# Performance work log

Hardware: AMD Instinct MI355X
Metric: run time of the kernel (lower is better)

## Reference

```python
import jax, jax.numpy as jnp
import numpy as np

B, T, I, H, O = 256, 2048, 6, 64, 6  # batch, time, input_dim, hidden_dim, output_dim


def setup_inputs() -> dict:
    key = jax.random.key(0)
    ks = jax.random.split(key, 11)
    s = 0.1  # param init scale
    return {
        "x": jax.random.normal(ks[0], (B, T, I), jnp.float32),
        # LSTM layer 0 (gate order i, f, g, o as in PyTorch; b = b_ih + b_hh)
        "Wih0": jax.random.normal(ks[1], (4 * H, I), jnp.float32) * s,
        "Whh0": jax.random.normal(ks[2], (4 * H, H), jnp.float32) * s,
        "b0": jax.random.normal(ks[3], (4 * H,), jnp.float32) * s,
        # LSTM layer 1
        "Wih1": jax.random.normal(ks[4], (4 * H, H), jnp.float32) * s,
        "Whh1": jax.random.normal(ks[5], (4 * H, H), jnp.float32) * s,
        "b1": jax.random.normal(ks[6], (4 * H,), jnp.float32) * s,
        # FC head
        "W1": jax.random.normal(ks[7], (H, H), jnp.float32) * s,
        "bf1": jax.random.normal(ks[8], (H,), jnp.float32) * s,
        "W2": jax.random.normal(ks[9], (O, H), jnp.float32) * s,
        "bf2": jax.random.normal(ks[10], (O,), jnp.float32) * s,
    }


def lstm_layer(x, Wih, Whh, b):
    """Single LSTM layer, batch_first. x: (B, T, F) -> (B, T, H)."""
    h_dim = Whh.shape[1]
    # precompute input contribution to gates for all timesteps: (B, T, 4H)
    xg = jnp.einsum('btf,gf->btg', x, Wih) + b

    def step(carry, xg_t):
        h, c = carry
        g = xg_t + h @ Whh.T                      # (B, 4H)
        i, f, gg, o = jnp.split(g, 4, axis=-1)    # PyTorch gate order i,f,g,o
        i = jax.nn.sigmoid(i)
        f = jax.nn.sigmoid(f)
        gg = jnp.tanh(gg)
        o = jax.nn.sigmoid(o)
        c = f * c + i * gg
        h = o * jnp.tanh(c)
        return (h, c), h

    h0 = jnp.zeros((x.shape[0], h_dim), x.dtype)
    _, hs = jax.lax.scan(step, (h0, h0), jnp.swapaxes(xg, 0, 1))  # (T, B, H)
    return jnp.swapaxes(hs, 0, 1)


def reference(x, Wih0, Whh0, b0, Wih1, Whh1, b1, W1, bf1, W2, bf2):
    h = lstm_layer(x, Wih0, Whh0, b0)
    h = lstm_layer(h, Wih1, Whh1, b1)   # eval mode: inter-layer dropout disabled
    h = jax.nn.relu(h @ W1.T + bf1)
    return h @ W2.T + bf2               # (B, T, O)
```

## Files before the change

### kernel.cpp

```cpp
#include <hip/hip_runtime.h>

#define TT 2048
#define HH 64
#define II 6
#define OO 6
#define NTHR 512

typedef float    f32x4 __attribute__((ext_vector_type(4)));
typedef float    f32x2 __attribute__((ext_vector_type(2)));
typedef _Float16 f16x8 __attribute__((ext_vector_type(8)));

__device__ __forceinline__ float fast_sig(float v) {
    return __builtin_amdgcn_rcpf(1.0f + __expf(-v));
}
__device__ __forceinline__ float fast_tanh(float v) {
    return 1.0f - 2.0f * __builtin_amdgcn_rcpf(__expf(2.0f * v) + 1.0f);
}

#define MFMA(a, b, c) __builtin_amdgcn_mfma_f32_16x16x32_f16((a), (b), (c), 0, 0, 0)

#define LGKM_BARRIER() asm volatile("s_waitcnt lgkmcnt(0)\ns_barrier" ::: "memory")

__global__
__attribute__((amdgpu_flat_work_group_size(NTHR, NTHR)))
__attribute__((amdgpu_waves_per_eu(2, 2)))
void lstm_mfma_kernel(const float* __restrict__ x,
                      const float* __restrict__ Wih0, const float* __restrict__ Whh0,
                      const float* __restrict__ b0,
                      const float* __restrict__ Wih1, const float* __restrict__ Whh1,
                      const float* __restrict__ b1,
                      const float* __restrict__ W1, const float* __restrict__ bf1,
                      const float* __restrict__ W2, const float* __restrict__ bf2,
                      float* __restrict__ out)
{
    const int row  = blockIdx.x;
    const int tid  = threadIdx.x;
    const int wid  = tid >> 6;
    const int lane = tid & 63;
    const int n    = lane & 15;
    const int q    = lane >> 4;
    const bool isA = wid < 4;
    const int  w   = isA ? wid : wid - 4;

    __shared__ __attribute__((aligned(16))) _Float16 H0[4][HH];
    __shared__ __attribute__((aligned(16))) _Float16 H1[2][HH];
    __shared__ __attribute__((aligned(16))) _Float16 Rb[2][HH];

    if (tid < HH) {
        H0[0][tid] = (_Float16)0.f; H0[1][tid] = (_Float16)0.f;
        H0[2][tid] = (_Float16)0.f; H0[3][tid] = (_Float16)0.f;
        H1[0][tid] = (_Float16)0.f; H1[1][tid] = (_Float16)0.f;
        Rb[0][tid] = (_Float16)0.f; Rb[1][tid] = (_Float16)0.f;
    }

    auto mk = [&](const float* W, int r, int ld, int kbase, int kmax, bool rok) {
        f16x8 f;
        #pragma unroll
        for (int i = 0; i < 8; ++i) {
            int kk = kbase + 8 * q + i;
            f[i] = (rok && kk < kmax) ? (_Float16)W[r * ld + kk] : (_Float16)0.f;
        }
        return f;
    };
    auto splat = [](float v) { f32x4 r = {v, v, v, v}; return r; };

    f16x8 frag[16], fragX[2];
    f32x4 biasv[4], biasX;
    const f32x4 zero4 = {0.f, 0.f, 0.f, 0.f};

    if (isA) {
        #pragma unroll
        for (int g = 0; g < 4; ++g) {
            const int r0 = g * HH + 16 * w + n;
            frag[g * 3 + 0] = mk(Whh0, r0, HH, 0,  HH, true);
            frag[g * 3 + 1] = mk(Whh0, r0, HH, 32, HH, true);
            frag[g * 3 + 2] = mk(Wih0, r0, II, 0,  II, true);
            biasv[g] = splat(b0[r0]);
        }
        const int rf = 16 * w + n;
        fragX[0] = mk(W1, rf, HH, 0,  HH, true);
        fragX[1] = mk(W1, rf, HH, 32, HH, true);
        biasX = splat(bf1[rf]);
        #pragma unroll
        for (int i = 12; i < 16; ++i) frag[i] = frag[0];
    } else {
        #pragma unroll
        for (int g = 0; g < 4; ++g) {
            const int r0 = g * HH + 16 * w + n;
            frag[g * 4 + 0] = mk(Wih1, r0, HH, 0,  HH, true);
            frag[g * 4 + 1] = mk(Wih1, r0, HH, 32, HH, true);
            frag[g * 4 + 2] = mk(Whh1, r0, HH, 0,  HH, true);
            frag[g * 4 + 3] = mk(Whh1, r0, HH, 32, HH, true);
            biasv[g] = splat(b1[r0]);
        }
        fragX[0] = mk(W2, n, HH, 0,  HH, n < OO);
        fragX[1] = mk(W2, n, HH, 32, HH, n < OO);
        biasX = splat((n < OO) ? bf2[n] : 0.f);
    }

    const float* xrow = x + (size_t)row * TT * II;
    {
        unsigned long long p = (unsigned long long)xrow;
        asm volatile("" : "+v"(p));
        xrow = (const float*)p;
    }
    f32x4 xc03 = {0.f, 0.f, 0.f, 0.f};
    f32x2 xc45 = {0.f, 0.f};
    if (isA) {
        xc03 = *reinterpret_cast<const f32x4*>(xrow);
        xc45 = *reinterpret_cast<const f32x2*>(xrow + 4);
    }

    float* outrow = out + (size_t)row * TT * OO;
    float cst = 0.f;

    __syncthreads();

    for (int t = 0; t <= TT + 3; ++t) {
        const int slp2 = (t + 1) & 1;
        const int slc2 = t & 1;

        if (isA) {
            const int tn = (t + 1 < TT) ? t + 1 : TT - 1;
            const float* xp = xrow + (size_t)tn * II;
            f32x4 xn03 = *reinterpret_cast<const f32x4*>(xp);
            f32x2 xn45 = *reinterpret_cast<const f32x2*>(xp + 4);

            const f16x8 a0  = *reinterpret_cast<const f16x8*>(&H0[(t + 3) & 3][8 * q]);
            const f16x8 a1  = *reinterpret_cast<const f16x8*>(&H0[(t + 3) & 3][32 + 8 * q]);
            const f16x8 b0f = *reinterpret_cast<const f16x8*>(&H1[slp2][8 * q]);
            const f16x8 b1f = *reinterpret_cast<const f16x8*>(&H1[slp2][32 + 8 * q]);
            f16x8 a2;
            a2[0] = (_Float16)xc03[0]; a2[1] = (_Float16)xc03[1];
            a2[2] = (_Float16)xc03[2]; a2[3] = (_Float16)xc03[3];
            a2[4] = (_Float16)xc45[0]; a2[5] = (_Float16)xc45[1];
            a2[6] = (_Float16)0.f;     a2[7] = (_Float16)0.f;

            float gv[4];
            #pragma unroll
            for (int g = 0; g < 4; ++g) {
                f32x4 acc0 = MFMA(a0, frag[g * 3 + 0], biasv[g]);
                f32x4 acc1 = MFMA(a1, frag[g * 3 + 1], zero4);
                f32x4 acc2 = MFMA(a2, frag[g * 3 + 2], zero4);
                gv[g] = (acc0[0] + acc1[0]) + acc2[0];
            }
            f32x4 f0 = MFMA(b0f, fragX[0], biasX);
            f32x4 f1 = MFMA(b1f, fragX[1], zero4);

            if (t < TT) {
                float i_ = fast_sig(gv[0]), f_ = fast_sig(gv[1]);
                float g_ = fast_tanh(gv[2]), o_ = fast_sig(gv[3]);
                cst = f_ * cst + i_ * g_;
                float h = o_ * fast_tanh(cst);
                if (lane < 16) H0[t & 3][16 * w + lane] = (_Float16)h;
            }
            {
                const int s3 = t - 3;
                if (s3 >= 0 && s3 < TT && lane < 16)
                    Rb[slp2][16 * w + lane] = (_Float16)fmaxf(f0[0] + f1[0], 0.f);
            }
            xc03 = xn03;
            xc45 = xn45;
        } else {
            const int s2 = t - 2, s4 = t - 4;
            const f16x8 h00 = *reinterpret_cast<const f16x8*>(&H0[(t + 2) & 3][8 * q]);
            const f16x8 h01 = *reinterpret_cast<const f16x8*>(&H0[(t + 2) & 3][32 + 8 * q]);
            const f16x8 a0  = *reinterpret_cast<const f16x8*>(&H1[slp2][8 * q]);
            const f16x8 a1  = *reinterpret_cast<const f16x8*>(&H1[slp2][32 + 8 * q]);
            const f16x8 r0  = *reinterpret_cast<const f16x8*>(&Rb[slc2][8 * q]);
            const f16x8 r1  = *reinterpret_cast<const f16x8*>(&Rb[slc2][32 + 8 * q]);

            float gv[4];
            #pragma unroll
            for (int g = 0; g < 4; ++g) {
                f32x4 acc0 = MFMA(h00, frag[g * 4 + 0], biasv[g]);
                f32x4 acc1 = MFMA(h01, frag[g * 4 + 1], zero4);
                f32x4 acc2 = MFMA(a0,  frag[g * 4 + 2], zero4);
                f32x4 acc3 = MFMA(a1,  frag[g * 4 + 3], zero4);
                gv[g] = (acc0[0] + acc1[0]) + (acc2[0] + acc3[0]);
            }
            f32x4 f0 = MFMA(r0, fragX[0], biasX);
            f32x4 f1 = MFMA(r1, fragX[1], zero4);

            if (s2 >= 0 && s2 < TT) {
                float i_ = fast_sig(gv[0]), f_ = fast_sig(gv[1]);
                float g_ = fast_tanh(gv[2]), o_ = fast_sig(gv[3]);
                cst = f_ * cst + i_ * g_;
                float h = o_ * fast_tanh(cst);
                if (lane < 16) H1[slc2][16 * w + lane] = (_Float16)h;
            }
            if (w == 0 && s4 >= 0 && s4 < TT && lane < OO)
                outrow[(size_t)s4 * OO + lane] = f0[0] + f1[0];
        }
        LGKM_BARRIER();
    }
}

extern "C" void kernel_launch(void* const* d_in, const int* in_sizes, int n_in,
                              void* d_out, int out_size, void* d_ws, size_t ws_size,
                              hipStream_t stream) {
    const float* xp   = (const float*)d_in[0];
    const float* Wih0 = (const float*)d_in[1];
    const float* Whh0 = (const float*)d_in[2];
    const float* b0   = (const float*)d_in[3];
    const float* Wih1 = (const float*)d_in[4];
    const float* Whh1 = (const float*)d_in[5];
    const float* b1   = (const float*)d_in[6];
    const float* W1   = (const float*)d_in[7];
    const float* bf1  = (const float*)d_in[8];
    const float* W2   = (const float*)d_in[9];
    const float* bf2  = (const float*)d_in[10];
    float* outp = (float*)d_out;

    lstm_mfma_kernel<<<dim3(256), dim3(NTHR), 0, stream>>>(
        xp, Wih0, Whh0, b0, Wih1, Whh1, b1, W1, bf1, W2, bf2, outp);
}
```

Before: 1.139 ms.

## Unroll LSTM time loop by four, rebalance FC head, compute input projection with FMAs

The time loop is split into checked prologue and epilogue steps plus a steady-state body unrolled by four, with constant LDS slot indices and no per-step bound checks. The layer-0 input projection moves from an MFMA with a half-empty fp16 fragment to six scalar fp32 FMAs per gate, and x is loaded in batches of four timesteps ahead of use. The W2 output head moves from layer-1 waves to wave 0 of the layer-0 group, so layer-1 waves run only their recurrent MFMAs. This aims to cut per-step instruction and branch overhead on the serial critical path, at the cost of more register pressure and extra work on the layer-0 waves.

Measured after the change: 1.167 ms. +2.4%, slower.

```diff
diff --git a/kernel.cpp b/kernel.cpp
--- a/kernel.cpp
+++ b/kernel.cpp
@@ -20,6 +20,63 @@
 #define MFMA(a, b, c) __builtin_amdgcn_mfma_f32_16x16x32_f16((a), (b), (c), 0, 0, 0)
 
 #define LGKM_BARRIER() asm volatile("s_waitcnt lgkmcnt(0)\ns_barrier" ::: "memory")
+
+#define STEP_STEADY(S, RP, WS, RPB, P1, P0)                                       \
+  {                                                                               \
+    if (isA) {                                                                    \
+      const f16x8 a0  = *reinterpret_cast<const f16x8*>(&H0[RP][8 * q]);          \
+      const f16x8 a1  = *reinterpret_cast<const f16x8*>(&H0[RP][32 + 8 * q]);     \
+      const f16x8 b0f = *reinterpret_cast<const f16x8*>(&H1[P1][8 * q]);          \
+      const f16x8 b1f = *reinterpret_cast<const f16x8*>(&H1[P1][32 + 8 * q]);     \
+      float gv[4];                                                                \
+      _Pragma("unroll")                                                           \
+      for (int g = 0; g < 4; ++g) {                                               \
+        f32x4 acc0 = MFMA(a0, fragG[2 * g + 0], zero4);                           \
+        f32x4 acc1 = MFMA(a1, fragG[2 * g + 1], zero4);                           \
+        float xd = b0j[g];                                                        \
+        _Pragma("unroll")                                                         \
+        for (int k2 = 0; k2 < 6; ++k2) xd = fmaf(wx[g][k2], xv[S][k2], xd);       \
+        gv[g] = (acc0[0] + acc1[0]) + xd;                                         \
+      }                                                                           \
+      f32x4 f0 = MFMA(b0f, fragX[0], biasX);                                      \
+      f32x4 f1 = MFMA(b1f, fragX[1], zero4);                                      \
+      if (w == 0) {                                                               \
+        const f16x8 r0 = *reinterpret_cast<const f16x8*>(&Rb[P0][8 * q]);         \
+        const f16x8 r1 = *reinterpret_cast<const f16x8*>(&Rb[P0][32 + 8 * q]);    \
+        f32x4 o0 = MFMA(r0, fragY[0], biasY);                                     \
+        f32x4 o1 = MFMA(r1, fragY[1], zero4);                                     \
+        if (lane < OO) op[OO * (S) + lane] = o0[0] + o1[0];                       \
+      }                                                                           \
+      float i_ = fast_sig(gv[0]), f_ = fast_sig(gv[1]);                           \
+      float g_ = fast_tanh(gv[2]), o_ = fast_sig(gv[3]);                          \
+      cst = f_ * cst + i_ * g_;                                                   \
+      float h = o_ * fast_tanh(cst);                                              \
+      if (lane < 16) {                                                            \
+        H0[WS][16 * w + lane] = (_Float16)h;                                      \
+        Rb[P1][16 * w + lane] = (_Float16)fmaxf(f0[0] + f1[0], 0.f);              \
+      }                                                                           \
+    } else {                                                                      \
+      const f16x8 h00 = *reinterpret_cast<const f16x8*>(&H0[RPB][8 * q]);         \
+      const f16x8 h01 = *reinterpret_cast<const f16x8*>(&H0[RPB][32 + 8 * q]);    \
+      const f16x8 a0  = *reinterpret_cast<const f16x8*>(&H1[P1][8 * q]);          \
+      const f16x8 a1  = *reinterpret_cast<const f16x8*>(&H1[P1][32 + 8 * q]);     \
+      float gv[4];                                                                \
+      _Pragma("unroll")                                                           \
+      for (int g = 0; g < 4; ++g) {                                               \
+        f32x4 acc0 = MFMA(h00, fragG[4 * g + 0], biasv[g]);                       \
+        f32x4 acc1 = MFMA(h01, fragG[4 * g + 1], zero4);                          \
+        f32x4 acc2 = MFMA(a0,  fragG[4 * g + 2], zero4);                          \
+        f32x4 acc3 = MFMA(a1,  fragG[4 * g + 3], zero4);                          \
+        gv[g] = (acc0[0] + acc1[0]) + (acc2[0] + acc3[0]);                        \
+      }                                                                           \
+      float i_ = fast_sig(gv[0]), f_ = fast_sig(gv[1]);                           \
+      float g_ = fast_tanh(gv[2]), o_ = fast_sig(gv[3]);                          \
+      cst = f_ * cst + i_ * g_;                                                   \
+      float h = o_ * fast_tanh(cst);                                              \
+      if (lane < 16) H1[P0][16 * w + lane] = (_Float16)h;                         \
+    }                                                                             \
+    LGKM_BARRIER();                                                               \
+  }
 
 __global__
 __attribute__((amdgpu_flat_work_group_size(NTHR, NTHR)))
@@ -64,38 +121,49 @@
     };
     auto splat = [](float v) { f32x4 r = {v, v, v, v}; return r; };
 
-    f16x8 frag[16], fragX[2];
-    f32x4 biasv[4], biasX;
+    f16x8 fragG[16], fragX[2], fragY[2];
+    f32x4 biasv[4], biasX, biasY;
+    float b0j[4];
+    float wx[4][6];
     const f32x4 zero4 = {0.f, 0.f, 0.f, 0.f};
 
     if (isA) {
         #pragma unroll
         for (int g = 0; g < 4; ++g) {
             const int r0 = g * HH + 16 * w + n;
-            frag[g * 3 + 0] = mk(Whh0, r0, HH, 0,  HH, true);
-            frag[g * 3 + 1] = mk(Whh0, r0, HH, 32, HH, true);
-            frag[g * 3 + 2] = mk(Wih0, r0, II, 0,  II, true);
-            biasv[g] = splat(b0[r0]);
-        }
+            fragG[2 * g + 0] = mk(Whh0, r0, HH, 0,  HH, true);
+            fragG[2 * g + 1] = mk(Whh0, r0, HH, 32, HH, true);
+            b0j[g] = b0[r0];
+            #pragma unroll
+            for (int k2 = 0; k2 < 6; ++k2) wx[g][k2] = Wih0[r0 * II + k2];
+        }
+        #pragma unroll
+        for (int i = 8; i < 16; ++i) fragG[i] = fragG[0];
         const int rf = 16 * w + n;
         fragX[0] = mk(W1, rf, HH, 0,  HH, true);
         fragX[1] = mk(W1, rf, HH, 32, HH, true);
         biasX = splat(bf1[rf]);
-        #pragma unroll
-        for (int i = 12; i < 16; ++i) frag[i] = frag[0];
+        fragY[0] = mk(W2, n, HH, 0,  HH, n < OO);
+        fragY[1] = mk(W2, n, HH, 32, HH, n < OO);
+        biasY = splat((n < OO) ? bf2[n] : 0.f);
+        #pragma unroll
+        for (int g = 0; g < 4; ++g) biasv[g] = zero4;
     } else {
         #pragma unroll
         for (int g = 0; g < 4; ++g) {
             const int r0 = g * HH + 16 * w + n;
-            frag[g * 4 + 0] = mk(Wih1, r0, HH, 0,  HH, true);
-            frag[g * 4 + 1] = mk(Wih1, r0, HH, 32, HH, true);
-            frag[g * 4 + 2] = mk(Whh1, r0, HH, 0,  HH, true);
-            frag[g * 4 + 3] = mk(Whh1, r0, HH, 32, HH, true);
+            fragG[4 * g + 0] = mk(Wih1, r0, HH, 0,  HH, true);
+            fragG[4 * g + 1] = mk(Wih1, r0, HH, 32, HH, true);
+            fragG[4 * g + 2] = mk(Whh1, r0, HH, 0,  HH, true);
+            fragG[4 * g + 3] = mk(Whh1, r0, HH, 32, HH, true);
             biasv[g] = splat(b1[r0]);
-        }
-        fragX[0] = mk(W2, n, HH, 0,  HH, n < OO);
-        fragX[1] = mk(W2, n, HH, 32, HH, n < OO);
-        biasX = splat((n < OO) ? bf2[n] : 0.f);
+            b0j[g] = 0.f;
+            #pragma unroll
+            for (int k2 = 0; k2 < 6; ++k2) wx[g][k2] = 0.f;
+        }
+        fragX[0] = fragG[0]; fragX[1] = fragG[1];
+        fragY[0] = fragG[0]; fragY[1] = fragG[1];
+        biasX = zero4; biasY = zero4;
     }
 
     const float* xrow = x + (size_t)row * TT * II;
@@ -104,96 +172,129 @@
         asm volatile("" : "+v"(p));
         xrow = (const float*)p;
     }
-    f32x4 xc03 = {0.f, 0.f, 0.f, 0.f};
-    f32x2 xc45 = {0.f, 0.f};
-    if (isA) {
-        xc03 = *reinterpret_cast<const f32x4*>(xrow);
-        xc45 = *reinterpret_cast<const f32x2*>(xrow + 4);
-    }
-
     float* outrow = out + (size_t)row * TT * OO;
+    float* op = nullptr;
+
+    float xv[5][6];
+    #pragma unroll
+    for (int s = 0; s < 5; ++s)
+        #pragma unroll
+        for (int k2 = 0; k2 < 6; ++k2) xv[s][k2] = 0.f;
+
     float cst = 0.f;
 
     __syncthreads();
 
-    for (int t = 0; t <= TT + 3; ++t) {
-        const int slp2 = (t + 1) & 1;
-        const int slc2 = t & 1;
-
+    auto step_checked = [&](int t) {
+        const int RP = (t + 3) & 3, WS = t & 3, RPB = (t + 2) & 3;
+        const int P1 = (t + 1) & 1, P0 = t & 1;
         if (isA) {
-            const int tn = (t + 1 < TT) ? t + 1 : TT - 1;
-            const float* xp = xrow + (size_t)tn * II;
-            f32x4 xn03 = *reinterpret_cast<const f32x4*>(xp);
-            f32x2 xn45 = *reinterpret_cast<const f32x2*>(xp + 4);
-
-            const f16x8 a0  = *reinterpret_cast<const f16x8*>(&H0[(t + 3) & 3][8 * q]);
-            const f16x8 a1  = *reinterpret_cast<const f16x8*>(&H0[(t + 3) & 3][32 + 8 * q]);
-            const f16x8 b0f = *reinterpret_cast<const f16x8*>(&H1[slp2][8 * q]);
-            const f16x8 b1f = *reinterpret_cast<const f16x8*>(&H1[slp2][32 + 8 * q]);
-            f16x8 a2;
-            a2[0] = (_Float16)xc03[0]; a2[1] = (_Float16)xc03[1];
-            a2[2] = (_Float16)xc03[2]; a2[3] = (_Float16)xc03[3];
-            a2[4] = (_Float16)xc45[0]; a2[5] = (_Float16)xc45[1];
-            a2[6] = (_Float16)0.f;     a2[7] = (_Float16)0.f;
-
+            const f16x8 a0  = *reinterpret_cast<const f16x8*>(&H0[RP][8 * q]);
+            const f16x8 a1  = *reinterpret_cast<const f16x8*>(&H0[RP][32 + 8 * q]);
+            const f16x8 b0f = *reinterpret_cast<const f16x8*>(&H1[P1][8 * q]);
+            const f16x8 b1f = *reinterpret_cast<const f16x8*>(&H1[P1][32 + 8 * q]);
+            float xs[6] = {0.f, 0.f, 0.f, 0.f, 0.f, 0.f};
+            if (t < TT) {
+                const float* xp = xrow + (size_t)t * II;
+                #pragma unroll
+                for (int k2 = 0; k2 < 6; ++k2) xs[k2] = xp[k2];
+            }
             float gv[4];
             #pragma unroll
             for (int g = 0; g < 4; ++g) {
-                f32x4 acc0 = MFMA(a0, frag[g * 3 + 0], biasv[g]);
-                f32x4 acc1 = MFMA(a1, frag[g * 3 + 1], zero4);
-                f32x4 acc2 = MFMA(a2, frag[g * 3 + 2], zero4);
-                gv[g] = (acc0[0] + acc1[0]) + acc2[0];
+                f32x4 acc0 = MFMA(a0, fragG[2 * g + 0], zero4);
+                f32x4 acc1 = MFMA(a1, fragG[2 * g + 1], zero4);
+                float xd = b0j[g];
+                #pragma unroll
+                for (int k2 = 0; k2 < 6; ++k2) xd = fmaf(wx[g][k2], xs[k2], xd);
+                gv[g] = (acc0[0] + acc1[0]) + xd;
             }
             f32x4 f0 = MFMA(b0f, fragX[0], biasX);
             f32x4 f1 = MFMA(b1f, fragX[1], zero4);
-
+            const int s4 = t - 4;
+            if (w == 0 && s4 >= 0 && s4 < TT) {
+                const f16x8 r0 = *reinterpret_cast<const f16x8*>(&Rb[P0][8 * q]);
+                const f16x8 r1 = *reinterpret_cast<const f16x8*>(&Rb[P0][32 + 8 * q]);
+                f32x4 o0 = MFMA(r0, fragY[0], biasY);
+                f32x4 o1 = MFMA(r1, fragY[1], zero4);
+                if (lane < OO) outrow[(size_t)s4 * OO + lane] = o0[0] + o1[0];
+            }
             if (t < TT) {
                 float i_ = fast_sig(gv[0]), f_ = fast_sig(gv[1]);
                 float g_ = fast_tanh(gv[2]), o_ = fast_sig(gv[3]);
                 cst = f_ * cst + i_ * g_;
                 float h = o_ * fast_tanh(cst);
-                if (lane < 16) H0[t & 3][16 * w + lane] = (_Float16)h;
-            }
-            {
-                const int s3 = t - 3;
-                if (s3 >= 0 && s3 < TT && lane < 16)
-                    Rb[slp2][16 * w + lane] = (_Float16)fmaxf(f0[0] + f1[0], 0.f);
-            }
-            xc03 = xn03;
-            xc45 = xn45;
+                if (lane < 16) H0[WS][16 * w + lane] = (_Float16)h;
+            }
+            const int s3 = t - 3;
+            if (s3 >= 0 && s3 < TT && lane < 16)
+                Rb[P1][16 * w + lane] = (_Float16)fmaxf(f0[0] + f1[0], 0.f);
         } else {
-            const int s2 = t - 2, s4 = t - 4;
-            const f16x8 h00 = *reinterpret_cast<const f16x8*>(&H0[(t + 2) & 3][8 * q]);
-            const f16x8 h01 = *reinterpret_cast<const f16x8*>(&H0[(t + 2) & 3][32 + 8 * q]);
-            const f16x8 a0  = *reinterpret_cast<const f16x8*>(&H1[slp2][8 * q]);
-            const f16x8 a1  = *reinterpret_cast<const f16x8*>(&H1[slp2][32 + 8 * q]);
-            const f16x8 r0  = *reinterpret_cast<const f16x8*>(&Rb[slc2][8 * q]);
-            const f16x8 r1  = *reinterpret_cast<const f16x8*>(&Rb[slc2][32 + 8 * q]);
-
+            const int s2 = t - 2;
+            const f16x8 h00 = *reinterpret_cast<const f16x8*>(&H0[RPB][8 * q]);
+            const f16x8 h01 = *reinterpret_cast<const f16x8*>(&H0[RPB][32 + 8 * q]);
+            const f16x8 a0  = *reinterpret_cast<const f16x8*>(&H1[P1][8 * q]);
+            const f16x8 a1  = *reinterpret_cast<const f16x8*>(&H1[P1][32 + 8 * q]);
             float gv[4];
             #pragma unroll
             for (int g = 0; g < 4; ++g) {
-                f32x4 acc0 = MFMA(h00, frag[g * 4 + 0], biasv[g]);
-                f32x4 acc1 = MFMA(h01, frag[g * 4 + 1], zero4);
-                f32x4 acc2 = MFMA(a0,  frag[g * 4 + 2], zero4);
-                f32x4 acc3 = MFMA(a1,  frag[g * 4 + 3], zero4);
+                f32x4 acc0 = MFMA(h00, fragG[4 * g + 0], biasv[g]);
+                f32x4 acc1 = MFMA(h01, fragG[4 * g + 1], zero4);
+                f32x4 acc2 = MFMA(a0,  fragG[4 * g + 2], zero4);
+                f32x4 acc3 = MFMA(a1,  fragG[4 * g + 3], zero4);
                 gv[g] = (acc0[0] + acc1[0]) + (acc2[0] + acc3[0]);
             }
-            f32x4 f0 = MFMA(r0, fragX[0], biasX);
-            f32x4 f1 = MFMA(r1, fragX[1], zero4);
-
             if (s2 >= 0 && s2 < TT) {
                 float i_ = fast_sig(gv[0]), f_ = fast_sig(gv[1]);
                 float g_ = fast_tanh(gv[2]), o_ = fast_sig(gv[3]);
                 cst = f_ * cst + i_ * g_;
                 float h = o_ * fast_tanh(cst);
-                if (lane < 16) H1[slc2][16 * w + lane] = (_Float16)h;
-            }
-            if (w == 0 && s4 >= 0 && s4 < TT && lane < OO)
-                outrow[(size_t)s4 * OO + lane] = f0[0] + f1[0];
+                if (lane < 16) H1[P0][16 * w + lane] = (_Float16)h;
+            }
         }
         LGKM_BARRIER();
-    }
+    };
+
+    for (int t = 0; t < 4; ++t) step_checked(t);
+
+    if (isA) {
+        const float* xp = xrow + (size_t)4 * II;
+        #pragma unroll
+        for (int k2 = 0; k2 < 6; ++k2) xv[0][k2] = xp[k2];
+    }
+
+    for (int tb = 4; tb <= TT - 8; tb += 4) {
+        if (isA) {
+            const float* xp = xrow + (size_t)tb * II;
+            f32x4 La = *reinterpret_cast<const f32x4*>(xp + 6);
+            f32x2 Lb = *reinterpret_cast<const f32x2*>(xp + 10);
+            f32x4 Ma = *reinterpret_cast<const f32x4*>(xp + 12);
+            f32x2 Mb = *reinterpret_cast<const f32x2*>(xp + 16);
+            f32x4 Na = *reinterpret_cast<const f32x4*>(xp + 18);
+            f32x2 Nb = *reinterpret_cast<const f32x2*>(xp + 22);
+            f32x4 Pa = *reinterpret_cast<const f32x4*>(xp + 24);
+            f32x2 Pb = *reinterpret_cast<const f32x2*>(xp + 28);
+            xv[1][0]=La[0]; xv[1][1]=La[1]; xv[1][2]=La[2]; xv[1][3]=La[3];
+            xv[1][4]=Lb[0]; xv[1][5]=Lb[1];
+            xv[2][0]=Ma[0]; xv[2][1]=Ma[1]; xv[2][2]=Ma[2]; xv[2][3]=Ma[3];
+            xv[2][4]=Mb[0]; xv[2][5]=Mb[1];
+            xv[3][0]=Na[0]; xv[3][1]=Na[1]; xv[3][2]=Na[2]; xv[3][3]=Na[3];
+            xv[3][4]=Nb[0]; xv[3][5]=Nb[1];
+            xv[4][0]=Pa[0]; xv[4][1]=Pa[1]; xv[4][2]=Pa[2]; xv[4][3]=Pa[3];
+            xv[4][4]=Pb[0]; xv[4][5]=Pb[1];
+            op = outrow + (size_t)(tb - 4) * OO;
+        }
+        STEP_STEADY(0, 3, 0, 2, 1, 0)
+        STEP_STEADY(1, 0, 1, 3, 0, 1)
+        STEP_STEADY(2, 1, 2, 0, 1, 0)
+        STEP_STEADY(3, 2, 3, 1, 0, 1)
+        if (isA) {
+            #pragma unroll
+            for (int k2 = 0; k2 < 6; ++k2) xv[0][k2] = xv[4][k2];
+        }
+    }
+
+    for (int t = TT - 4; t <= TT + 3; ++t) step_checked(t);
 }
 
 extern "C" void kernel_launch(void* const* d_in, const int* in_sizes, int n_in,
```

## Split LSTM pipeline into four wave roles to shorten per-step critical path

Applied to the files above, without the earlier changes.

Doubles the workgroup to 16 waves and gives each group of four waves one role: the layer-0 recurrence, the layer-1 input projection, the layer-1 recurrence, and the FC head. The layer-1 input projection is computed one step ahead and handed over through a double-buffered shared XG array. The layer-0 input term becomes six scalar FMAs instead of a padded MFMA. Together these cut the MFMA chain each wave runs between barriers. The cost is a 16-wave barrier every timestep, one more pipeline stage of shared-memory traffic, and the occupancy hint raised to 4 waves per EU, which limits registers per wave.

After: 1.450 ms. +27.2%, slower.

```diff
diff --git a/kernel.cpp b/kernel.cpp
--- a/kernel.cpp
+++ b/kernel.cpp
@@ -4,7 +4,7 @@
 #define HH 64
 #define II 6
 #define OO 6
-#define NTHR 512
+#define NTHR 1024
 
 typedef float    f32x4 __attribute__((ext_vector_type(4)));
 typedef float    f32x2 __attribute__((ext_vector_type(2)));
@@ -23,7 +23,7 @@
 
 __global__
 __attribute__((amdgpu_flat_work_group_size(NTHR, NTHR)))
-__attribute__((amdgpu_waves_per_eu(2, 2)))
+__attribute__((amdgpu_waves_per_eu(4, 4)))
 void lstm_mfma_kernel(const float* __restrict__ x,
                       const float* __restrict__ Wih0, const float* __restrict__ Whh0,
                       const float* __restrict__ b0,
@@ -39,19 +39,20 @@
     const int lane = tid & 63;
     const int n    = lane & 15;
     const int q    = lane >> 4;
-    const bool isA = wid < 4;
-    const int  w   = isA ? wid : wid - 4;
-
-    __shared__ __attribute__((aligned(16))) _Float16 H0[4][HH];
+    const int role = wid >> 2;
+    const int w    = wid & 3;
+
+    __shared__ __attribute__((aligned(16))) _Float16 H0[2][HH];
     __shared__ __attribute__((aligned(16))) _Float16 H1[2][HH];
     __shared__ __attribute__((aligned(16))) _Float16 Rb[2][HH];
+    __shared__ __attribute__((aligned(16))) float    XG[2][4 * HH];
 
     if (tid < HH) {
         H0[0][tid] = (_Float16)0.f; H0[1][tid] = (_Float16)0.f;
-        H0[2][tid] = (_Float16)0.f; H0[3][tid] = (_Float16)0.f;
         H1[0][tid] = (_Float16)0.f; H1[1][tid] = (_Float16)0.f;
         Rb[0][tid] = (_Float16)0.f; Rb[1][tid] = (_Float16)0.f;
     }
+    if (tid < 2 * 4 * HH) XG[0][tid] = 0.f;
 
     auto mk = [&](const float* W, int r, int ld, int kbase, int kmax, bool rok) {
         f16x8 f;
@@ -63,39 +64,60 @@
         return f;
     };
     auto splat = [](float v) { f32x4 r = {v, v, v, v}; return r; };
-
-    f16x8 frag[16], fragX[2];
-    f32x4 biasv[4], biasX;
     const f32x4 zero4 = {0.f, 0.f, 0.f, 0.f};
 
-    if (isA) {
+    f16x8 fragG[8], fragX[2], fragY[2];
+    f32x4 biasv[4], biasX = zero4, biasY = zero4;
+    float b0j[4] = {0.f, 0.f, 0.f, 0.f};
+    float wx[4][6];
+    #pragma unroll
+    for (int g = 0; g < 4; ++g) {
+        biasv[g] = zero4;
+        #pragma unroll
+        for (int k2 = 0; k2 < 6; ++k2) wx[g][k2] = 0.f;
+    }
+
+    if (role == 0) {
         #pragma unroll
         for (int g = 0; g < 4; ++g) {
             const int r0 = g * HH + 16 * w + n;
-            frag[g * 3 + 0] = mk(Whh0, r0, HH, 0,  HH, true);
-            frag[g * 3 + 1] = mk(Whh0, r0, HH, 32, HH, true);
-            frag[g * 3 + 2] = mk(Wih0, r0, II, 0,  II, true);
-            biasv[g] = splat(b0[r0]);
-        }
+            fragG[2 * g + 0] = mk(Whh0, r0, HH, 0,  HH, true);
+            fragG[2 * g + 1] = mk(Whh0, r0, HH, 32, HH, true);
+            b0j[g] = b0[r0];
+            #pragma unroll
+            for (int k2 = 0; k2 < 6; ++k2) wx[g][k2] = Wih0[r0 * II + k2];
+        }
+        fragX[0] = fragG[0]; fragX[1] = fragG[1];
+        fragY[0] = fragG[0]; fragY[1] = fragG[1];
+    } else if (role == 1) {
+        #pragma unroll
+        for (int g = 0; g < 4; ++g) {
+            const int r0 = g * HH + 16 * w + n;
+            fragG[2 * g + 0] = mk(Wih1, r0, HH, 0,  HH, true);
+            fragG[2 * g + 1] = mk(Wih1, r0, HH, 32, HH, true);
+            biasv[g] = splat(b1[r0]);
+        }
+        fragX[0] = fragG[0]; fragX[1] = fragG[1];
+        fragY[0] = fragG[0]; fragY[1] = fragG[1];
+    } else if (role == 2) {
+        #pragma unroll
+        for (int g = 0; g < 4; ++g) {
+            const int r0 = g * HH + 16 * w + n;
+            fragG[2 * g + 0] = mk(Whh1, r0, HH, 0,  HH, true);
+            fragG[2 * g + 1] = mk(Whh1, r0, HH, 32, HH, true);
+        }
+        fragX[0] = fragG[0]; fragX[1] = fragG[1];
+        fragY[0] = fragG[0]; fragY[1] = fragG[1];
+    } else {
         const int rf = 16 * w + n;
         fragX[0] = mk(W1, rf, HH, 0,  HH, true);
         fragX[1] = mk(W1, rf, HH, 32, HH, true);
         biasX = splat(bf1[rf]);
-        #pragma unroll
-        for (int i = 12; i < 16; ++i) frag[i] = frag[0];
-    } else {
-        #pragma unroll
-        for (int g = 0; g < 4; ++g) {
-            const int r0 = g * HH + 16 * w + n;
-            frag[g * 4 + 0] = mk(Wih1, r0, HH, 0,  HH, true);
-            frag[g * 4 + 1] = mk(Wih1, r0, HH, 32, HH, true);
-            frag[g * 4 + 2] = mk(Whh1, r0, HH, 0,  HH, true);
-            frag[g * 4 + 3] = mk(Whh1, r0, HH, 32, HH, true);
-            biasv[g] = splat(b1[r0]);
-        }
-        fragX[0] = mk(W2, n, HH, 0,  HH, n < OO);
-        fragX[1] = mk(W2, n, HH, 32, HH, n < OO);
-        biasX = splat((n < OO) ? bf2[n] : 0.f);
+        fragY[0] = mk(W2, n, HH, 0,  HH, n < OO);
+        fragY[1] = mk(W2, n, HH, 32, HH, n < OO);
+        biasY = splat((n < OO) ? bf2[n] : 0.f);
+        #pragma unroll
+        for (int i = 0; i < 8; ++i) fragG[i] = fragX[0];
     }
 
     const float* xrow = x + (size_t)row * TT * II;
@@ -106,7 +128,7 @@
     }
     f32x4 xc03 = {0.f, 0.f, 0.f, 0.f};
     f32x2 xc45 = {0.f, 0.f};
-    if (isA) {
+    if (role == 0) {
         xc03 = *reinterpret_cast<const f32x4*>(xrow);
         xc45 = *reinterpret_cast<const f32x2*>(xrow + 4);
     }
@@ -117,80 +139,82 @@
     __syncthreads();
 
     for (int t = 0; t <= TT + 3; ++t) {
-        const int slp2 = (t + 1) & 1;
-        const int slc2 = t & 1;
-
-        if (isA) {
+        const int sp = (t + 1) & 1;
+        const int sc = t & 1;
+
+        if (role == 0) {
             const int tn = (t + 1 < TT) ? t + 1 : TT - 1;
             const float* xp = xrow + (size_t)tn * II;
             f32x4 xn03 = *reinterpret_cast<const f32x4*>(xp);
             f32x2 xn45 = *reinterpret_cast<const f32x2*>(xp + 4);
 
-            const f16x8 a0  = *reinterpret_cast<const f16x8*>(&H0[(t + 3) & 3][8 * q]);
-            const f16x8 a1  = *reinterpret_cast<const f16x8*>(&H0[(t + 3) & 3][32 + 8 * q]);
-            const f16x8 b0f = *reinterpret_cast<const f16x8*>(&H1[slp2][8 * q]);
-            const f16x8 b1f = *reinterpret_cast<const f16x8*>(&H1[slp2][32 + 8 * q]);
-            f16x8 a2;
-            a2[0] = (_Float16)xc03[0]; a2[1] = (_Float16)xc03[1];
-            a2[2] = (_Float16)xc03[2]; a2[3] = (_Float16)xc03[3];
-            a2[4] = (_Float16)xc45[0]; a2[5] = (_Float16)xc45[1];
-            a2[6] = (_Float16)0.f;     a2[7] = (_Float16)0.f;
-
+            const f16x8 a0 = *reinterpret_cast<const f16x8*>(&H0[sp][8 * q]);
+            const f16x8 a1 = *reinterpret_cast<const f16x8*>(&H0[sp][32 + 8 * q]);
             float gv[4];
             #pragma unroll
             for (int g = 0; g < 4; ++g) {
-                f32x4 acc0 = MFMA(a0, frag[g * 3 + 0], biasv[g]);
-                f32x4 acc1 = MFMA(a1, frag[g * 3 + 1], zero4);
-                f32x4 acc2 = MFMA(a2, frag[g * 3 + 2], zero4);
-                gv[g] = (acc0[0] + acc1[0]) + acc2[0];
-            }
-            f32x4 f0 = MFMA(b0f, fragX[0], biasX);
-            f32x4 f1 = MFMA(b1f, fragX[1], zero4);
-
+                f32x4 acc0 = MFMA(a0, fragG[2 * g + 0], zero4);
+                f32x4 acc1 = MFMA(a1, fragG[2 * g + 1], zero4);
+                float xd = b0j[g];
+                xd = fmaf(wx[g][0], xc03[0], xd); xd = fmaf(wx[g][1], xc03[1], xd);
+                xd = fmaf(wx[g][2], xc03[2], xd); xd = fmaf(wx[g][3], xc03[3], xd);
+                xd = fmaf(wx[g][4], xc45[0], xd); xd = fmaf(wx[g][5], xc45[1], xd);
+                gv[g] = (acc0[0] + acc1[0]) + xd;
+            }
             if (t < TT) {
                 float i_ = fast_sig(gv[0]), f_ = fast_sig(gv[1]);
                 float g_ = fast_tanh(gv[2]), o_ = fast_sig(gv[3]);
                 cst = f_ * cst + i_ * g_;
                 float h = o_ * fast_tanh(cst);
-                if (lane < 16) H0[t & 3][16 * w + lane] = (_Float16)h;
-            }
-            {
-                const int s3 = t - 3;
-                if (s3 >= 0 && s3 < TT && lane < 16)
-                    Rb[slp2][16 * w + lane] = (_Float16)fmaxf(f0[0] + f1[0], 0.f);
+                if (lane < 16) H0[sc][16 * w + lane] = (_Float16)h;
             }
             xc03 = xn03;
             xc45 = xn45;
-        } else {
-            const int s2 = t - 2, s4 = t - 4;
-            const f16x8 h00 = *reinterpret_cast<const f16x8*>(&H0[(t + 2) & 3][8 * q]);
-            const f16x8 h01 = *reinterpret_cast<const f16x8*>(&H0[(t + 2) & 3][32 + 8 * q]);
-            const f16x8 a0  = *reinterpret_cast<const f16x8*>(&H1[slp2][8 * q]);
-            const f16x8 a1  = *reinterpret_cast<const f16x8*>(&H1[slp2][32 + 8 * q]);
-            const f16x8 r0  = *reinterpret_cast<const f16x8*>(&Rb[slc2][8 * q]);
-            const f16x8 r1  = *reinterpret_cast<const f16x8*>(&Rb[slc2][32 + 8 * q]);
-
+        } else if (role == 1) {
+            const f16x8 a0 = *reinterpret_cast<const f16x8*>(&H0[sp][8 * q]);
+            const f16x8 a1 = *reinterpret_cast<const f16x8*>(&H0[sp][32 + 8 * q]);
+            #pragma unroll
+            for (int g = 0; g < 4; ++g) {
+                f32x4 acc0 = MFMA(a0, fragG[2 * g + 0], biasv[g]);
+                f32x4 acc1 = MFMA(a1, fragG[2 * g + 1], zero4);
+                if (t >= 1 && t <= TT && lane < 16)
+                    XG[sp][g * HH + 16 * w + lane] = acc0[0] + acc1[0];
+            }
+        } else if (role == 2) {
+            const int s2 = t - 2;
+            const f16x8 a0 = *reinterpret_cast<const f16x8*>(&H1[sp][8 * q]);
+            const f16x8 a1 = *reinterpret_cast<const f16x8*>(&H1[sp][32 + 8 * q]);
             float gv[4];
             #pragma unroll
             for (int g = 0; g < 4; ++g) {
-                f32x4 acc0 = MFMA(h00, frag[g * 4 + 0], biasv[g]);
-                f32x4 acc1 = MFMA(h01, frag[g * 4 + 1], zero4);
-                f32x4 acc2 = MFMA(a0,  frag[g * 4 + 2], zero4);
-                f32x4 acc3 = MFMA(a1,  frag[g * 4 + 3], zero4);
-                gv[g] = (acc0[0] + acc1[0]) + (acc2[0] + acc3[0]);
-            }
-            f32x4 f0 = MFMA(r0, fragX[0], biasX);
-            f32x4 f1 = MFMA(r1, fragX[1], zero4);
-
+                const float xgv = XG[sc][g * HH + 16 * w + n];
+                f32x4 acc0 = MFMA(a0, fragG[2 * g + 0], zero4);
+                f32x4 acc1 = MFMA(a1, fragG[2 * g + 1], zero4);
+                gv[g] = (acc0[0] + acc1[0]) + xgv;
+            }
             if (s2 >= 0 && s2 < TT) {
                 float i_ = fast_sig(gv[0]), f_ = fast_sig(gv[1]);
                 float g_ = fast_tanh(gv[2]), o_ = fast_sig(gv[3]);
                 cst = f_ * cst + i_ * g_;
                 float h = o_ * fast_tanh(cst);
-                if (lane < 16) H1[slc2][16 * w + lane] = (_Float16)h;
-            }
-            if (w == 0 && s4 >= 0 && s4 < TT && lane < OO)
-                outrow[(size_t)s4 * OO + lane] = f0[0] + f1[0];
+                if (lane < 16) H1[sc][16 * w + lane] = (_Float16)h;
+            }
+        } else {
+            const int s3 = t - 3, s4 = t - 4;
+            const f16x8 a0 = *reinterpret_cast<const f16x8*>(&H1[sp][8 * q]);
+            const f16x8 a1 = *reinterpret_cast<const f16x8*>(&H1[sp][32 + 8 * q]);
+            f32x4 f0 = MFMA(a0, fragX[0], biasX);
+            f32x4 f1 = MFMA(a1, fragX[1], zero4);
+            if (s3 >= 0 && s3 < TT && lane < 16)
+                Rb[sp][16 * w + lane] = (_Float16)fmaxf(f0[0] + f1[0], 0.f);
+            if (w == 0) {
+                const f16x8 r0 = *reinterpret_cast<const f16x8*>(&Rb[sc][8 * q]);
+                const f16x8 r1 = *reinterpret_cast<const f16x8*>(&Rb[sc][32 + 8 * q]);
+                f32x4 o0 = MFMA(r0, fragY[0], biasY);
+                f32x4 o1 = MFMA(r1, fragY[1], zero4);
+                if (s4 >= 0 && s4 < TT && lane < OO)
+                    outrow[(size_t)s4 * OO + lane] = o0[0] + o1[0];
+            }
         }
         LGKM_BARRIER();
     }
```
